# Kernel optimization log

Hardware: AMD Instinct MI355X
Metric: run time of the kernel (lower is better)

Reference implementation:

```python
import jax, jax.numpy as jnp
import numpy as np

N, E, B_GRAPHS = 50000, 512000, 64
XD, ED, C, H, L = 16, 8, 64, 2, 2
EPS = 1e-5


def setup_inputs() -> dict:
    key = jax.random.key(0)
    ks = jax.random.split(key, 20)
    w = lambda k, shape: jax.random.normal(k, shape, jnp.float32) * 0.1
    return {
        "x": jax.random.normal(ks[0], (N, XD), jnp.float32),
        "edge_attr": jax.random.normal(ks[1], (E, ED), jnp.float32),
        "edge_src": jax.random.randint(ks[2], (E,), 0, N, dtype=jnp.int32),
        "edge_dst": jax.random.randint(ks[3], (E,), 0, N, dtype=jnp.int32),
        "batch": jnp.sort(jax.random.randint(ks[4], (N,), 0, B_GRAPHS, dtype=jnp.int32)),
        "node_W": w(ks[5], (XD, C)), "node_b": jnp.zeros((C,), jnp.float32),
        "edge_W": w(ks[6], (ED, C)), "edge_b": jnp.zeros((C,), jnp.float32),
        "Wq": w(ks[7], (L, C, H * C)), "bq": jnp.zeros((L, H * C), jnp.float32),
        "Wk": w(ks[8], (L, C, H * C)), "bk": jnp.zeros((L, H * C), jnp.float32),
        "Wv": w(ks[9], (L, C, H * C)), "bv": jnp.zeros((L, H * C), jnp.float32),
        "We": w(ks[10], (L, C, H * C)), "be": jnp.zeros((L, H * C), jnp.float32),
        "Wskip": w(ks[11], (L, C, C)), "bskip": jnp.zeros((L, C), jnp.float32),
        "gamma": jnp.ones((L, C), jnp.float32), "beta": jnp.zeros((L, C), jnp.float32),
        "gate_W": w(ks[12], (C, 1)), "gate_b": jnp.zeros((1,), jnp.float32),
        "out_W": w(ks[13], (C, 1)), "out_b": jnp.zeros((1,), jnp.float32),
    }


def reference(x, edge_attr, edge_src, edge_dst, batch,
              node_W, node_b, edge_W, edge_b,
              Wq, bq, Wk, bk, Wv, bv, We, be,
              Wskip, bskip, gamma, beta,
              gate_W, gate_b, out_W, out_b):
    n = x.shape[0]
    h = x @ node_W + node_b                       # node encoder: [N, C]
    e = edge_attr @ edge_W + edge_b               # edge encoder: [E, C]
    scale = 1.0 / jnp.sqrt(jnp.float32(C))
    for i in range(L):
        identity = h
        # TransformerConv (UniMP), concat=False -> mean over heads
        q = (h @ Wq[i] + bq[i]).reshape(n, H, C)
        k = (h @ Wk[i] + bk[i]).reshape(n, H, C)
        v = (h @ Wv[i] + bv[i]).reshape(n, H, C)
        ep = (e @ We[i] + be[i]).reshape(-1, H, C)
        k_e = k[edge_src] + ep                    # [E, H, C]
        v_e = v[edge_src] + ep                    # [E, H, C]
        logits = jnp.einsum('ehc,ehc->eh', q[edge_dst], k_e) * scale
        # segment softmax over incoming edges of each target node
        m = jax.ops.segment_max(logits, edge_dst, num_segments=n)
        a = jnp.exp(logits - m[edge_dst])
        denom = jax.ops.segment_sum(a, edge_dst, num_segments=n)
        alpha = a / denom[edge_dst]               # [E, H]
        agg = jax.ops.segment_sum(alpha[:, :, None] * v_e, edge_dst, num_segments=n)
        out = agg.mean(axis=1) + h @ Wskip[i] + bskip[i]   # root/skip term
        # BatchNorm1d (training mode, biased variance)
        mu = out.mean(axis=0)
        var = out.var(axis=0)
        out = gamma[i] * (out - mu) * jax.lax.rsqrt(var + EPS) + beta[i]
        out = jax.nn.leaky_relu(out, 0.01)
        h = out + identity                        # residual
    # GlobalAttention pooling over graphs
    gate = (h @ gate_W + gate_b)[:, 0]            # [N]
    gm = jax.ops.segment_max(gate, batch, num_segments=B_GRAPHS)
    ge = jnp.exp(gate - gm[batch])
    gd = jax.ops.segment_sum(ge, batch, num_segments=B_GRAPHS)
    wts = ge / gd[batch]
    pooled = jax.ops.segment_sum(wts[:, None] * h, batch, num_segments=B_GRAPHS)
    return jax.nn.sigmoid(pooled @ out_W + out_b)  # [B_GRAPHS, 1]
```

## Files before the change

kernel.cpp:

```cpp
#include <hip/hip_runtime.h>
#include <hip/hip_bf16.h>

typedef unsigned short ushort_t;
typedef __attribute__((ext_vector_type(8))) short short8;
typedef __attribute__((ext_vector_type(4))) float float4v;

__device__ __forceinline__ float bfu_lo(unsigned u) {
    return __uint_as_float(u << 16);
}
__device__ __forceinline__ float bfu_hi(unsigned u) {
    return __uint_as_float(u & 0xffff0000u);
}
__device__ __forceinline__ ushort_t f2bf(float f) {
    __hip_bfloat16 h = __float2bfloat16(f);
    return *reinterpret_cast<ushort_t*>(&h);
}



__global__ __launch_bounds__(256) void setup_kernel(
    const float* __restrict__ x, const float* __restrict__ node_W,
    const float* __restrict__ node_b,
    const float* __restrict__ edge_W, const float* __restrict__ edge_b,
    const float* __restrict__ We, const float* __restrict__ be,
    const float* __restrict__ Wq, const float* __restrict__ bq,
    const float* __restrict__ Wk, const float* __restrict__ bk,
    const float* __restrict__ Wv, const float* __restrict__ bv,
    const float* __restrict__ Wskip, const float* __restrict__ bskip,
    float* __restrict__ h, ushort_t* __restrict__ h_bf,
    int* __restrict__ counts,
    float* __restrict__ Wc, float* __restrict__ bcb,
    ushort_t* __restrict__ Wall_arr, float* __restrict__ Wall_bias,
    ushort_t* __restrict__ wv_arr,
    int O0, int O1, int O2, int N) {
    int b = blockIdx.x, t = threadIdx.x;
    if (b < O0) {
        int idx = b * 256 + t;
        if (idx < N * 64) {
            int n = idx >> 6, c = idx & 63;
            float acc = node_b[c];
#pragma unroll
            for (int j = 0; j < 16; ++j) acc += x[n * 16 + j] * node_W[j * 64 + c];
            h[idx] = acc;
            h_bf[idx] = f2bf(acc);
        }
    } else if (b < O1) {
        int i = (b - O0) * 256 + t;
        if (i < N) counts[i] = 0;
    } else if (b < O2) {
        int tid = (b - O1) * 256 + t;
        if (tid < 2048) {
            int l = tid >> 10, d = (tid >> 7) & 7, j = tid & 127;
            float s = 0.f;
            for (int m = 0; m < 64; ++m) s += edge_W[d * 64 + m] * We[l * 8192 + m * 128 + j];
            Wc[l * 1024 + d * 128 + j] = s;
        } else if (tid < 2048 + 256) {
            int u = tid - 2048;
            int l = u >> 7, j = u & 127;
            float s = be[l * 128 + j];
            for (int m = 0; m < 64; ++m) s += edge_b[m] * We[l * 8192 + m * 128 + j];
            bcb[l * 128 + j] = s;
        }
    } else {
        int tid = (b - O2) * 256 + t;
        if (tid < 2 * 14336) {
            int l = tid / 14336, u = tid % 14336;
            int j = u & 7, ln = (u >> 3) & 63, kch = (u >> 9) & 1, ct = u >> 10;
            int nn = ln & 15, quad = ln >> 4;
            int k = kch * 32 + quad * 8 + j;
            int col = ct * 16 + nn;
            float v = 0.f;
            if (col < 128) {
                int hh = col >> 6, m = col & 63;
                const float* wq = Wq + l * 8192 + k * 128 + hh * 64;
                const float* wk = Wk + l * 8192 + m * 128 + hh * 64;
                float s = 0.f;
                for (int c2 = 0; c2 < 64; ++c2) s += wq[c2] * wk[c2];
                v = 0.125f * s;
            } else if (col < 192) {
                v = Wskip[l * 4096 + k * 64 + (col - 128)];
            }
            Wall_arr[(size_t)l * 14336 + ct * 1024 + kch * 512 + ln * 8 + j] = f2bf(v);
        } else if (tid < 2 * 14336 + 2 * 224) {
            int u = tid - 2 * 14336;
            int l = u / 224, col = u % 224;
            float v = 0.f;
            if (col < 128) {
                int hh = col >> 6, m = col & 63;
                const float* bqp = bq + l * 128 + hh * 64;
                const float* wk = Wk + l * 8192 + m * 128 + hh * 64;
                float s = 0.f;
                for (int c2 = 0; c2 < 64; ++c2) s += bqp[c2] * wk[c2];
                v = 0.125f * s;
            } else if (col < 192) {
                v = bskip[l * 64 + col - 128];
            }
            Wall_bias[l * 224 + col] = v;
        } else if (tid < 2 * 14336 + 2 * 224 + 2 * 8192) {
            int u = tid - (2 * 14336 + 2 * 224);
            int l = u >> 13, r = u & 8191;
            int j = r & 7, ln = (r >> 3) & 63, ct = (r >> 9) & 3, kc = r >> 11;
            int quad = ln >> 4, nn = ln & 15;
            int p = kc * 32 + quad * 8 + j;
            int hh = p >> 6, m = p & 63;
            int c2 = ct * 16 + nn;
            wv_arr[(size_t)l * 8192 + r] = f2bf(Wv[l * 8192 + m * 128 + hh * 64 + c2]);
        }
    }
}

__global__ void combine2_kernel(const float* __restrict__ Wq, const float* __restrict__ bq,
                                const float* __restrict__ bk, const float* __restrict__ bv,
                                const float* __restrict__ Wc, const float* __restrict__ bcb,
                                ushort_t* __restrict__ Wall_arr, float* __restrict__ Wall_bias,
                                float* __restrict__ cst) {
    int tid = blockIdx.x * 256 + threadIdx.x;
    if (tid < 2304) {
        int l = tid / 1152, u = tid % 1152, k = u / 18, j = u % 18;
        float s = 0.f;
        if (j < 16) {
            int hh = j >> 3, d = j & 7;
            for (int c = 0; c < 64; ++c)
                s += Wq[l * 8192 + k * 128 + hh * 64 + c] * Wc[l * 1024 + d * 128 + hh * 64 + c];
        } else {
            int hh = j - 16;
            for (int c = 0; c < 64; ++c)
                s += Wq[l * 8192 + k * 128 + hh * 64 + c] *
                     (bcb[l * 128 + hh * 64 + c] + bk[l * 128 + hh * 64 + c]);
        }
        s *= 0.125f;
        int col = 192 + j;
        int ct = col >> 4, nn = col & 15;
        int kch = k >> 5, quad = (k >> 3) & 3, jj = k & 7;
        int ln = quad * 16 + nn;
        Wall_arr[(size_t)l * 14336 + ct * 1024 + kch * 512 + ln * 8 + jj] = f2bf(s);
    } else if (tid < 2304 + 36) {
        int u = tid - 2304;
        int l = u / 18, j = u % 18;
        float s = 0.f;
        if (j < 16) {
            int hh = j >> 3, d = j & 7;
            for (int c = 0; c < 64; ++c)
                s += bq[l * 128 + hh * 64 + c] * Wc[l * 1024 + d * 128 + hh * 64 + c];
        } else {
            int hh = j - 16;
            for (int c = 0; c < 64; ++c)
                s += bq[l * 128 + hh * 64 + c] *
                     (bcb[l * 128 + hh * 64 + c] + bk[l * 128 + hh * 64 + c]);
        }
        Wall_bias[l * 224 + 192 + j] = 0.125f * s;
    } else if (tid < 2304 + 36 + 128) {
        int u = tid - 2340;
        int l = u >> 6, c = u & 63;
        cst[l * 64 + c] = 0.5f * (bv[l * 128 + c] + bv[l * 128 + 64 + c] +
                                  bcb[l * 128 + c] + bcb[l * 128 + 64 + c]);
    }
}


__global__ void csr_count_kernel(const int* __restrict__ dst, int* __restrict__ counts, int E) {
    int e = blockIdx.x * 256 + threadIdx.x;
    if (e < E) atomicAdd(&counts[dst[e]], 1);
}

__global__ void scan1_kernel(const int* __restrict__ counts, int* __restrict__ rowptr,
                             int* __restrict__ bsums, int N) {
    __shared__ int s[256];
    int t = threadIdx.x, i = blockIdx.x * 256 + t;
    int v = (i < N) ? counts[i] : 0;
    s[t] = v;
    __syncthreads();
    for (int d = 1; d < 256; d <<= 1) {
        int x = (t >= d) ? s[t - d] : 0;
        __syncthreads();
        s[t] += x;
        __syncthreads();
    }
    if (i < N) rowptr[i] = s[t] - v;
    if (t == 255) bsums[blockIdx.x] = s[255];
}

__global__ void scan3_kernel(int* __restrict__ rowptr, const int* __restrict__ bsums,
                             int* __restrict__ cursor, int N, int E, int nb) {
    __shared__ int sh[256];
    int t = threadIdx.x;
    int v = (t < nb) ? bsums[t] : 0;
    sh[t] = v;
    __syncthreads();
    for (int d = 1; d < 256; d <<= 1) {
        int x = (t >= d) ? sh[t - d] : 0;
        __syncthreads();
        sh[t] += x;
        __syncthreads();
    }
    int blk = blockIdx.x;
    int offv = (blk == 0) ? 0 : sh[blk - 1];
    int i = blk * 256 + t;
    if (i < N) {
        int r = rowptr[i] + offv;
        rowptr[i] = r;
        cursor[i] = r;
    }
    if (i == 0) rowptr[N] = E;
}

__global__ void csr_fill_kernel(const int* __restrict__ dst, const int* __restrict__ src,
                                const float* __restrict__ edge_attr, int* __restrict__ cursor,
                                char* __restrict__ erec, int E) {
    int e = blockIdx.x * 256 + threadIdx.x;
    if (e < E) {
        int pos = atomicAdd(&cursor[dst[e]], 1);
        float4 a0 = *(const float4*)(edge_attr + (size_t)e * 8);
        float4 a1 = *(const float4*)(edge_attr + (size_t)e * 8 + 4);
        uint4 w1;
        w1.x = (unsigned)f2bf(a0.x) | ((unsigned)f2bf(a0.y) << 16);
        w1.y = (unsigned)f2bf(a0.z) | ((unsigned)f2bf(a0.w) << 16);
        w1.z = (unsigned)f2bf(a1.x) | ((unsigned)f2bf(a1.y) << 16);
        w1.w = (unsigned)f2bf(a1.z) | ((unsigned)f2bf(a1.w) << 16);
        char* rp = erec + (size_t)pos * 32;
        *(uint4*)rp = make_uint4((unsigned)(src[e] * 128), 0u, 0u, 0u);
        *(uint4*)(rp + 16) = w1;
    }
}


__global__ __launch_bounds__(512) void layer_kernel(
    const ushort_t* __restrict__ h_bf,
    const char* __restrict__ erec, const int* __restrict__ rowptr,
    const ushort_t* __restrict__ Wall_arr, const float* __restrict__ Wall_bias,
    const ushort_t* __restrict__ wv_arr, const float* __restrict__ Wc,
    const float* __restrict__ cst,
    float* __restrict__ outbuf, float* __restrict__ part, int N) {
    __shared__ ushort_t qk2_s[32][128];
    __shared__ ushort_t ha_s[32][136];
    __shared__ float qc_s[32][20];
    __shared__ float skip_s[32][64];
    __shared__ float sen_s[32][16];
    __shared__ float dw_s[32];
    __shared__ float Wc_s[1024];
    __shared__ float cst_s[64];
    __shared__ float ps[2][128];
    int t = threadIdx.x;
    int lane = t & 63, wid = t >> 6;
    int n0 = blockIdx.x * 32;
    for (int i = t; i < 1024; i += 512) Wc_s[i] = Wc[i];
    if (t < 64) cst_s[t] = cst[t];

    {
        int quad = lane >> 4, nn16 = lane & 15;
        int nodeA = n0 + nn16;      if (nodeA >= N) nodeA = N - 1;
        int nodeB = n0 + 16 + nn16; if (nodeB >= N) nodeB = N - 1;
        const ushort_t* apA = h_bf + (size_t)nodeA * 64 + quad * 8;
        const ushort_t* apB = h_bf + (size_t)nodeB * 64 + quad * 8;
        short8 aA0 = *(const short8*)apA;
        short8 aA1 = *(const short8*)(apA + 32);
        short8 aB0 = *(const short8*)apB;
        short8 aB1 = *(const short8*)(apB + 32);
        for (int ct = wid; ct < 14; ct += 8) {
            const ushort_t* bp = Wall_arr + (size_t)ct * 1024 + lane * 8;
            short8 b0 = *(const short8*)bp;
            short8 b1 = *(const short8*)(bp + 512);
            float4v cA = {0.f, 0.f, 0.f, 0.f};
            float4v cB = {0.f, 0.f, 0.f, 0.f};
            cA = __builtin_amdgcn_mfma_f32_16x16x32_bf16(aA0, b0, cA, 0, 0, 0);
            cA = __builtin_amdgcn_mfma_f32_16x16x32_bf16(aA1, b1, cA, 0, 0, 0);
            cB = __builtin_amdgcn_mfma_f32_16x16x32_bf16(aB0, b0, cB, 0, 0, 0);
            cB = __builtin_amdgcn_mfma_f32_16x16x32_bf16(aB1, b1, cB, 0, 0, 0);
            int col = ct * 16 + nn16;
            float bias = Wall_bias[col];
#pragma unroll
            for (int g = 0; g < 2; ++g) {
                float4v c = g ? cB : cA;
                int lbase = g * 16 + quad * 4;
#pragma unroll
                for (int r = 0; r < 4; ++r) {
                    float v = c[r] + bias;
                    int ln2 = lbase + r;
                    if (col < 128) qk2_s[ln2][col] = f2bf(v);
                    else if (col < 192) skip_s[ln2][col - 128] = v;
                    else if (col < 210) qc_s[ln2][col - 192] = v;
                }
            }
        }
    }
    __syncthreads();

    {
        int grp = lane >> 4, l16 = lane & 15;
        int head = l16 >> 3, l8 = l16 & 7;
        const char* hbb = (const char*)h_bf;
        int ln = wid * 4 + grp;
        int n = n0 + ln;
        bool active = (n < N);
        int nn = active ? n : (N - 1);
        int start = rowptr[nn];
        int deg = active ? (rowptr[nn + 1] - start) : 0;
        int wdeg = deg;
        wdeg = max(wdeg, __shfl_xor(wdeg, 16));
        wdeg = max(wdeg, __shfl_xor(wdeg, 32));

        float lsum = 0.f;
        float hacc[8] = {0.f, 0.f, 0.f, 0.f, 0.f, 0.f, 0.f, 0.f};
        float se[8]   = {0.f, 0.f, 0.f, 0.f, 0.f, 0.f, 0.f, 0.f};

        if (wdeg > 0) {
            uint4 qr = *(const uint4*)&qk2_s[ln][head * 64 + l8 * 8];
            float qk0 = bfu_lo(qr.x), qk1 = bfu_hi(qr.x);
            float qk2f = bfu_lo(qr.y), qk3 = bfu_hi(qr.y);
            float qk4 = bfu_lo(qr.z), qk5 = bfu_hi(qr.z);
            float qk6 = bfu_lo(qr.w), qk7 = bfu_hi(qr.w);
            float4 qcA = *(const float4*)&qc_s[ln][head * 8];
            float4 qcB = *(const float4*)&qc_s[ln][head * 8 + 4];
            float qb = qc_s[ln][16 + head];

            bool dpos = (deg > 0);
            int dclamp = dpos ? (deg - 1) : 0;

            int offL = *(const int*)(erec + (size_t)(dpos ? (start + min(l16, dclamp)) : 0) * 32);
            int o0 = __shfl(offL, grp * 16);
            uint4 ca = *(const uint4*)(hbb + (size_t)(unsigned)o0 + l8 * 16);
            int gi0 = dpos ? start : 0;
            uint4 ev = *(const uint4*)(erec + (size_t)gi0 * 32 + 16);

            for (int it = 0; it < wdeg; ++it) {
                int itn = it + 1;
                if ((itn & 15) == 0)
                    offL = *(const int*)(erec +
                            (size_t)(dpos ? (start + min(itn + l16, dclamp)) : 0) * 32);
                int itc = min(itn, wdeg - 1);
                int on = __shfl(offL, grp * 16 + (itc & 15));
                uint4 na = *(const uint4*)(hbb + (size_t)(unsigned)on + l8 * 16);
                int gin = dpos ? (start + min(itc, dclamp)) : 0;
                uint4 fv = *(const uint4*)(erec + (size_t)gin * 32 + 16);

                float h0 = bfu_lo(ca.x), h1 = bfu_hi(ca.x);
                float h2 = bfu_lo(ca.y), h3 = bfu_hi(ca.y);
                float h4 = bfu_lo(ca.z), h5 = bfu_hi(ca.z);
                float h6 = bfu_lo(ca.w), h7 = bfu_hi(ca.w);
                float dt = qk0 * h0 + qk1 * h1 + qk2f * h2 + qk3 * h3
                         + qk4 * h4 + qk5 * h5 + qk6 * h6 + qk7 * h7;
                dt += __shfl_xor(dt, 1);
                dt += __shfl_xor(dt, 2);
                dt += __shfl_xor(dt, 4);
                float ex0 = bfu_lo(ev.x), ex1 = bfu_hi(ev.x);
                float ex2 = bfu_lo(ev.y), ex3 = bfu_hi(ev.y);
                float ex4 = bfu_lo(ev.z), ex5 = bfu_hi(ev.z);
                float ex6 = bfu_lo(ev.w), ex7 = bfu_hi(ev.w);
                float s0 = dt
                         + qcA.x * ex0 + qcA.y * ex1 + qcA.z * ex2 + qcA.w * ex3
                         + qcB.x * ex4 + qcB.y * ex5 + qcB.z * ex6 + qcB.w * ex7
                         + qb;
                float p = (it < deg) ? __expf(fmaxf(s0, -60.f)) : 0.f;
                lsum += p;
                hacc[0] += p * h0; hacc[1] += p * h1;
                hacc[2] += p * h2; hacc[3] += p * h3;
                hacc[4] += p * h4; hacc[5] += p * h5;
                hacc[6] += p * h6; hacc[7] += p * h7;
                se[0] += p * ex0; se[1] += p * ex1; se[2] += p * ex2; se[3] += p * ex3;
                se[4] += p * ex4; se[5] += p * ex5; se[6] += p * ex6; se[7] += p * ex7;
                ca = na; ev = fv;
            }
        }

        float inv = (deg > 0) ? (0.5f / lsum) : 0.f;
#pragma unroll
        for (int j2 = 0; j2 < 8; ++j2)
            ha_s[ln][head * 64 + l8 * 8 + j2] = f2bf(hacc[j2] * inv);
        if (l8 == 0) {
#pragma unroll
            for (int m = 0; m < 8; ++m) sen_s[ln][head * 8 + m] = se[m] * inv;
            if (head == 0) dw_s[ln] = (deg > 0) ? 1.f : 0.f;
        }
    }
    __syncthreads();

    {
        int quad = lane >> 4, nn16 = lane & 15;
        int ct = wid & 3, g = wid >> 2;
        float4v c = {0.f, 0.f, 0.f, 0.f};
#pragma unroll
        for (int kc = 0; kc < 4; ++kc) {
            short8 a = *(const short8*)&ha_s[g * 16 + nn16][kc * 32 + quad * 8];
            short8 b = *(const short8*)(wv_arr + kc * 2048 + ct * 512 + lane * 8);
            c = __builtin_amdgcn_mfma_f32_16x16x32_bf16(a, b, c, 0, 0, 0);
        }
        int col = ct * 16 + nn16;
        float sa = 0.f, sq = 0.f;
#pragma unroll
        for (int r = 0; r < 4; ++r) {
            int ln2 = g * 16 + quad * 4 + r;
            int nr = n0 + ln2;
            const float* sp = sen_s[ln2];
            float ep = 0.f;
#pragma unroll
            for (int hh = 0; hh < 2; ++hh)
#pragma unroll
                for (int d = 0; d < 8; ++d)
                    ep += sp[hh * 8 + d] * Wc_s[d * 128 + hh * 64 + col];
            if (nr < N) {
                float val = c[r] + ep + dw_s[ln2] * cst_s[col] + skip_s[ln2][col];
                outbuf[(size_t)nr * 64 + col] = val;
                sa += val;
                sq += val * val;
            }
        }
        sa += __shfl_xor(sa, 16); sa += __shfl_xor(sa, 32);
        sq += __shfl_xor(sq, 16); sq += __shfl_xor(sq, 32);
        if (quad == 0) { ps[g][col] = sa; ps[g][64 + col] = sq; }
    }
    __syncthreads();
    if (t < 128) part[(size_t)blockIdx.x * 128 + t] = ps[0][t] + ps[1][t];
}


__global__ __launch_bounds__(256) void bnreduce_kernel(const float* __restrict__ part,
                                                       float* __restrict__ bnsums, int nb) {
    int s = blockIdx.x;
    int t = threadIdx.x;
    float a = 0.f;
    for (int b = t; b < nb; b += 256) a += part[(size_t)b * 128 + s];
    __shared__ float sh[256];
    sh[t] = a;
    __syncthreads();
    for (int d = 128; d; d >>= 1) {
        if (t < d) sh[t] += sh[t + d];
        __syncthreads();
    }
    if (t == 0) bnsums[s] = sh[0];
}

__global__ __launch_bounds__(256) void bnh_kernel(
    const float* __restrict__ outbuf, const float* __restrict__ bnsums,
    const float* __restrict__ gamma, const float* __restrict__ beta,
    float* __restrict__ h, ushort_t* __restrict__ h_bf, int N) {
    int idx = blockIdx.x * 256 + threadIdx.x;
    if (idx >= N * 64) return;
    int c = idx & 63;
    float invN = 1.f / (float)N;
    float mean = bnsums[c] * invN;
    float var = bnsums[64 + c] * invN - mean * mean;
    float scale = gamma[c] * rsqrtf(var + 1e-5f);
    float shift = beta[c] - mean * scale;
    float o = outbuf[idx] * scale + shift;
    o = (o > 0.f) ? o : 0.01f * o;
    float hn = h[idx] + o;
    h[idx] = hn;
    h_bf[idx] = f2bf(hn);
}

__global__ __launch_bounds__(256) void bnapply_kernel(
    const float* __restrict__ outbuf, const float* __restrict__ bnsums,
    const float* __restrict__ gamma, const float* __restrict__ beta,
    const float* __restrict__ gate_W, const float* __restrict__ gate_b,
    float* __restrict__ h, float* __restrict__ gatebuf, int N) {
    int idx = blockIdx.x * 256 + threadIdx.x;
    if (idx >= N * 64) return;
    int c = idx & 63, n = idx >> 6;
    float invN = 1.f / (float)N;
    float mean = bnsums[c] * invN;
    float var = bnsums[64 + c] * invN - mean * mean;
    float scale = gamma[c] * rsqrtf(var + 1e-5f);
    float shift = beta[c] - mean * scale;
    float o = outbuf[idx] * scale + shift;
    o = (o > 0.f) ? o : 0.01f * o;
    float hn = h[idx] + o;
    h[idx] = hn;
    float g = hn * gate_W[c];
#pragma unroll
    for (int off = 32; off; off >>= 1) g += __shfl_xor(g, off);
    if (c == 0) gatebuf[n] = g + gate_b[0];
}


__global__ __launch_bounds__(256) void pool_acc_kernel(
    const float* __restrict__ h, const float* __restrict__ gatebuf,
    const int* __restrict__ batch,
    float* __restrict__ pacc, float* __restrict__ pden, int N) {
    int b = blockIdx.x >> 3, chunk = blockIdx.x & 7;
    int lo = 0, hi = N;
    while (lo < hi) { int mid = (lo + hi) >> 1; if (batch[mid] < b) lo = mid + 1; else hi = mid; }
    int start = lo;
    lo = start; hi = N;
    while (lo < hi) { int mid = (lo + hi) >> 1; if (batch[mid] <= b) lo = mid + 1; else hi = mid; }
    int end = lo;
    int t = threadIdx.x, lane = t & 63, wid = t >> 6;
    __shared__ float sm[4];
    float mx = -1e30f;
    for (int n = start + t; n < end; n += 256) mx = fmaxf(mx, gatebuf[n]);
#pragma unroll
    for (int off = 32; off; off >>= 1) mx = fmaxf(mx, __shfl_xor(mx, off));
    if (lane == 0) sm[wid] = mx;
    __syncthreads();
    float mb = fmaxf(fmaxf(sm[0], sm[1]), fmaxf(sm[2], sm[3]));
    int gwid = chunk * 4 + wid;
    float acc = 0.f, den = 0.f;
    for (int n = start + gwid; n < end; n += 32) {
        float ge = __expf(gatebuf[n] - mb);
        acc += ge * h[(size_t)n * 64 + lane];
        den += ge;
    }
    __shared__ float sacc[4][64];
    __shared__ float sden[4];
    sacc[wid][lane] = acc;
    if (lane == 0) sden[wid] = den;
    __syncthreads();
    if (wid == 0) {
        pacc[(size_t)blockIdx.x * 64 + lane] =
            sacc[0][lane] + sacc[1][lane] + sacc[2][lane] + sacc[3][lane];
        if (lane == 0) pden[blockIdx.x] = sden[0] + sden[1] + sden[2] + sden[3];
    }
}

__global__ void pool_fin_kernel(const float* __restrict__ pacc, const float* __restrict__ pden,
                                const float* __restrict__ out_W, const float* __restrict__ out_b,
                                float* __restrict__ out) {
    int b = blockIdx.x, c = threadIdx.x;
    float pc = 0.f, dv = 0.f;
#pragma unroll
    for (int j = 0; j < 8; ++j) {
        pc += pacc[(size_t)(b * 8 + j) * 64 + c];
        dv += pden[b * 8 + j];
    }
    float s = pc * out_W[c];
#pragma unroll
    for (int off = 32; off; off >>= 1) s += __shfl_xor(s, off);
    if (c == 0) {
        if (dv <= 0.f) dv = 1.f;
        float v = s / dv + out_b[0];
        out[b] = 1.f / (1.f + __expf(-v));
    }
}


extern "C" void kernel_launch(void* const* d_in, const int* in_sizes, int n_in,
                              void* d_out, int out_size, void* d_ws, size_t ws_size,
                              hipStream_t stream) {
    const float* x         = (const float*)d_in[0];
    const float* edge_attr = (const float*)d_in[1];
    const int*   edge_src  = (const int*)d_in[2];
    const int*   edge_dst  = (const int*)d_in[3];
    const int*   batch     = (const int*)d_in[4];
    const float* node_W    = (const float*)d_in[5];
    const float* node_b    = (const float*)d_in[6];
    const float* edge_W    = (const float*)d_in[7];
    const float* edge_b    = (const float*)d_in[8];
    const float* Wq        = (const float*)d_in[9];
    const float* bq        = (const float*)d_in[10];
    const float* Wk        = (const float*)d_in[11];
    const float* bk        = (const float*)d_in[12];
    const float* Wv        = (const float*)d_in[13];
    const float* bv        = (const float*)d_in[14];
    const float* We        = (const float*)d_in[15];
    const float* be        = (const float*)d_in[16];
    const float* Wskip     = (const float*)d_in[17];
    const float* bskip     = (const float*)d_in[18];
    const float* gamma     = (const float*)d_in[19];
    const float* beta      = (const float*)d_in[20];
    const float* gate_W    = (const float*)d_in[21];
    const float* gate_b    = (const float*)d_in[22];
    const float* out_W     = (const float*)d_in[23];
    const float* out_b     = (const float*)d_in[24];
    float* out = (float*)d_out;

    const int N = in_sizes[0] / 16;
    const int E = in_sizes[2];
    const int nbv = (N + 31) / 32;

    char* ws = (char*)d_ws;
    size_t off = 0;
    auto alloc = [&](size_t bytes) {
        size_t o = off;
        off += (bytes + 255) & ~(size_t)255;
        return o;
    };
    float*    h        = (float*)(ws + alloc((size_t)N * 64 * 4));
    ushort_t* h_bf     = (ushort_t*)(ws + alloc((size_t)N * 64 * 2));
    float*    outbuf   = (float*)(ws + alloc((size_t)N * 64 * 4));
    int*      rowptr   = (int*)(ws + alloc((size_t)(N + 1) * 4));
    int*      cursor   = (int*)(ws + alloc((size_t)N * 4));
    int*      counts   = (int*)(ws + alloc((size_t)N * 4));
    int*      bsums    = (int*)(ws + alloc(1024));
    char*     erec     = (char*)(ws + alloc((size_t)E * 32));
    float*    Wc       = (float*)(ws + alloc(2 * 1024 * 4));
    float*    bcb      = (float*)(ws + alloc(2 * 128 * 4));
    ushort_t* Wall_arr = (ushort_t*)(ws + alloc(2 * 14336 * 2));
    float*    Wall_b   = (float*)(ws + alloc(2 * 224 * 4));
    ushort_t* wv_arr   = (ushort_t*)(ws + alloc(2 * 8192 * 2));
    float*    cst      = (float*)(ws + alloc(2 * 64 * 4));
    float*    bnsums   = (float*)(ws + alloc(128 * 4));
    float*    gatebuf  = (float*)(ws + alloc((size_t)N * 4));
    float*    part     = (float*)(ws + alloc((size_t)nbv * 128 * 4));
    float*    pacc     = (float*)(ws + alloc((size_t)512 * 64 * 4));
    float*    pden     = (float*)(ws + alloc(512 * 4));
    if (off > ws_size) return;

    int O0 = (N * 64 + 255) / 256;
    int O1 = O0 + (N + 255) / 256;
    int O2 = O1 + 9;
    int O3 = O2 + 178;
    setup_kernel<<<O3, 256, 0, stream>>>(
        x, node_W, node_b, edge_W, edge_b, We, be, Wq, bq, Wk, bk, Wv, bv, Wskip, bskip,
        h, h_bf, counts, Wc, bcb, Wall_arr, Wall_b, wv_arr, O0, O1, O2, N);
    combine2_kernel<<<10, 256, 0, stream>>>(Wq, bq, bk, bv, Wc, bcb, Wall_arr, Wall_b, cst);

    csr_count_kernel<<<(E + 255) / 256, 256, 0, stream>>>(edge_dst, counts, E);
    int nb = (N + 255) / 256;
    scan1_kernel<<<nb, 256, 0, stream>>>(counts, rowptr, bsums, N);
    scan3_kernel<<<nb, 256, 0, stream>>>(rowptr, bsums, cursor, N, E, nb);
    csr_fill_kernel<<<(E + 255) / 256, 256, 0, stream>>>(edge_dst, edge_src, edge_attr,
                                                         cursor, erec, E);

    layer_kernel<<<nbv, 512, 0, stream>>>(h_bf, erec, rowptr,
                                          Wall_arr, Wall_b, wv_arr, Wc, cst,
                                          outbuf, part, N);
    bnreduce_kernel<<<128, 256, 0, stream>>>(part, bnsums, nbv);
    bnh_kernel<<<(N * 64 + 255) / 256, 256, 0, stream>>>(
        outbuf, bnsums, gamma, beta, h, h_bf, N);

    layer_kernel<<<nbv, 512, 0, stream>>>(h_bf, erec, rowptr,
                                          Wall_arr + 14336, Wall_b + 224, wv_arr + 8192,
                                          Wc + 1024, cst + 64,
                                          outbuf, part, N);
    bnreduce_kernel<<<128, 256, 0, stream>>>(part, bnsums, nbv);
    bnapply_kernel<<<(N * 64 + 255) / 256, 256, 0, stream>>>(
        outbuf, bnsums, gamma + 64, beta + 64, gate_W, gate_b, h, gatebuf, N);

    pool_acc_kernel<<<512, 256, 0, stream>>>(h, gatebuf, batch, pacc, pden, N);
    pool_fin_kernel<<<64, 64, 0, stream>>>(pacc, pden, out_W, out_b, out);
}
```

Baseline: 341.5 us.

## Split each node's incoming edges across two warps, halving nodes per block

The layer kernel now handles 16 nodes per 512-thread block instead of 32, and each node's edge list is split between a pair of wavefronts. Each half accumulates partial softmax sums and weighted features, which are merged through shared memory before normalization. This shortens the serial per-node edge loop, evens out load across degrees, and doubles the block count. The cost is an extra barrier and shared-memory reduction, less reuse of the projection weights per block, and only half the waves taking part in the final MFMA stage.

```diff
diff --git a/kernel.cpp b/kernel.cpp
--- a/kernel.cpp
+++ b/kernel.cpp
@@ -231,55 +231,46 @@
     const ushort_t* __restrict__ wv_arr, const float* __restrict__ Wc,
     const float* __restrict__ cst,
     float* __restrict__ outbuf, float* __restrict__ part, int N) {
-    __shared__ ushort_t qk2_s[32][128];
-    __shared__ ushort_t ha_s[32][136];
-    __shared__ float qc_s[32][20];
-    __shared__ float skip_s[32][64];
-    __shared__ float sen_s[32][16];
-    __shared__ float dw_s[32];
+    __shared__ ushort_t qk2_s[16][128];
+    __shared__ ushort_t ha_s[16][136];
+    __shared__ float qc_s[16][20];
+    __shared__ float skip_s[16][64];
+    __shared__ float sen_s[16][16];
+    __shared__ float dw_s[16];
     __shared__ float Wc_s[1024];
     __shared__ float cst_s[64];
-    __shared__ float ps[2][128];
+    __shared__ float ps[128];
+    __shared__ float ph[16][128];
+    __shared__ float pse[16][16];
+    __shared__ float plsum[16][2];
     int t = threadIdx.x;
     int lane = t & 63, wid = t >> 6;
-    int n0 = blockIdx.x * 32;
+    int n0 = blockIdx.x * 16;
     for (int i = t; i < 1024; i += 512) Wc_s[i] = Wc[i];
     if (t < 64) cst_s[t] = cst[t];
 
     {
         int quad = lane >> 4, nn16 = lane & 15;
-        int nodeA = n0 + nn16;      if (nodeA >= N) nodeA = N - 1;
-        int nodeB = n0 + 16 + nn16; if (nodeB >= N) nodeB = N - 1;
+        int nodeA = n0 + nn16; if (nodeA >= N) nodeA = N - 1;
         const ushort_t* apA = h_bf + (size_t)nodeA * 64 + quad * 8;
-        const ushort_t* apB = h_bf + (size_t)nodeB * 64 + quad * 8;
         short8 aA0 = *(const short8*)apA;
         short8 aA1 = *(const short8*)(apA + 32);
-        short8 aB0 = *(const short8*)apB;
-        short8 aB1 = *(const short8*)(apB + 32);
         for (int ct = wid; ct < 14; ct += 8) {
             const ushort_t* bp = Wall_arr + (size_t)ct * 1024 + lane * 8;
             short8 b0 = *(const short8*)bp;
             short8 b1 = *(const short8*)(bp + 512);
             float4v cA = {0.f, 0.f, 0.f, 0.f};
-            float4v cB = {0.f, 0.f, 0.f, 0.f};
             cA = __builtin_amdgcn_mfma_f32_16x16x32_bf16(aA0, b0, cA, 0, 0, 0);
             cA = __builtin_amdgcn_mfma_f32_16x16x32_bf16(aA1, b1, cA, 0, 0, 0);
-            cB = __builtin_amdgcn_mfma_f32_16x16x32_bf16(aB0, b0, cB, 0, 0, 0);
-            cB = __builtin_amdgcn_mfma_f32_16x16x32_bf16(aB1, b1, cB, 0, 0, 0);
             int col = ct * 16 + nn16;
             float bias = Wall_bias[col];
 #pragma unroll
-            for (int g = 0; g < 2; ++g) {
-                float4v c = g ? cB : cA;
-                int lbase = g * 16 + quad * 4;
-#pragma unroll
-                for (int r = 0; r < 4; ++r) {
-                    float v = c[r] + bias;
-                    int ln2 = lbase + r;
-                    if (col < 128) qk2_s[ln2][col] = f2bf(v);
-                    else if (col < 192) skip_s[ln2][col - 128] = v;
-                    else if (col < 210) qc_s[ln2][col - 192] = v;
-                }
+            for (int r = 0; r < 4; ++r) {
+                float v = cA[r] + bias;
+                int ln2 = quad * 4 + r;
+                if (col < 128) qk2_s[ln2][col] = f2bf(v);
+                else if (col < 192) skip_s[ln2][col - 128] = v;
+                else if (col < 210) qc_s[ln2][col - 192] = v;
             }
         }
     }
@@ -288,14 +279,18 @@
     {
         int grp = lane >> 4, l16 = lane & 15;
         int head = l16 >> 3, l8 = l16 & 7;
+        int pairIdx = wid >> 1, halfIdx = wid & 1;
         const char* hbb = (const char*)h_bf;
-        int ln = wid * 4 + grp;
+        int ln = pairIdx * 4 + grp;
         int n = n0 + ln;
         bool active = (n < N);
         int nn = active ? n : (N - 1);
         int start = rowptr[nn];
         int deg = active ? (rowptr[nn + 1] - start) : 0;
-        int wdeg = deg;
+        int h1cnt = (deg + 1) >> 1;
+        int mycnt = halfIdx ? (deg - h1cnt) : h1cnt;
+        int mystart = start + (halfIdx ? h1cnt : 0);
+        int wdeg = mycnt;
         wdeg = max(wdeg, __shfl_xor(wdeg, 16));
         wdeg = max(wdeg, __shfl_xor(wdeg, 32));
 
@@ -313,24 +308,23 @@
             float4 qcB = *(const float4*)&qc_s[ln][head * 8 + 4];
             float qb = qc_s[ln][16 + head];
 
-            bool dpos = (deg > 0);
-            int dclamp = dpos ? (deg - 1) : 0;
-
-            int offL = *(const int*)(erec + (size_t)(dpos ? (start + min(l16, dclamp)) : 0) * 32);
+            bool dpos = (mycnt > 0);
+            int dclamp = dpos ? (mycnt - 1) : 0;
+            int base = dpos ? mystart : 0;
+
+            int offL = *(const int*)(erec + (size_t)(base + min(l16, dclamp)) * 32);
             int o0 = __shfl(offL, grp * 16);
             uint4 ca = *(const uint4*)(hbb + (size_t)(unsigned)o0 + l8 * 16);
-            int gi0 = dpos ? start : 0;
-            uint4 ev = *(const uint4*)(erec + (size_t)gi0 * 32 + 16);
+            uint4 ev = *(const uint4*)(erec + (size_t)base * 32 + 16);
 
             for (int it = 0; it < wdeg; ++it) {
                 int itn = it + 1;
                 if ((itn & 15) == 0)
-                    offL = *(const int*)(erec +
-                            (size_t)(dpos ? (start + min(itn + l16, dclamp)) : 0) * 32);
+                    offL = *(const int*)(erec + (size_t)(base + min(itn + l16, dclamp)) * 32);
                 int itc = min(itn, wdeg - 1);
                 int on = __shfl(offL, grp * 16 + (itc & 15));
                 uint4 na = *(const uint4*)(hbb + (size_t)(unsigned)on + l8 * 16);
-                int gin = dpos ? (start + min(itc, dclamp)) : 0;
+                int gin = base + min(itc, dclamp);
                 uint4 fv = *(const uint4*)(erec + (size_t)gin * 32 + 16);
 
                 float h0 = bfu_lo(ca.x), h1 = bfu_hi(ca.x);
@@ -350,7 +344,7 @@
                          + qcA.x * ex0 + qcA.y * ex1 + qcA.z * ex2 + qcA.w * ex3
                          + qcB.x * ex4 + qcB.y * ex5 + qcB.z * ex6 + qcB.w * ex7
                          + qb;
-                float p = (it < deg) ? __expf(fmaxf(s0, -60.f)) : 0.f;
+                float p = (it < mycnt) ? __expf(fmaxf(s0, -60.f)) : 0.f;
                 lsum += p;
                 hacc[0] += p * h0; hacc[1] += p * h1;
                 hacc[2] += p * h2; hacc[3] += p * h3;
@@ -362,25 +356,41 @@
             }
         }
 
-        float inv = (deg > 0) ? (0.5f / lsum) : 0.f;
-#pragma unroll
-        for (int j2 = 0; j2 < 8; ++j2)
-            ha_s[ln][head * 64 + l8 * 8 + j2] = f2bf(hacc[j2] * inv);
-        if (l8 == 0) {
-#pragma unroll
-            for (int m = 0; m < 8; ++m) sen_s[ln][head * 8 + m] = se[m] * inv;
-            if (head == 0) dw_s[ln] = (deg > 0) ? 1.f : 0.f;
-        }
-    }
-    __syncthreads();
-
-    {
+        if (halfIdx == 1) {
+#pragma unroll
+            for (int j2 = 0; j2 < 8; ++j2) ph[ln][head * 64 + l8 * 8 + j2] = hacc[j2];
+            if (l8 == 0) {
+#pragma unroll
+                for (int m = 0; m < 8; ++m) pse[ln][head * 8 + m] = se[m];
+                plsum[ln][head] = lsum;
+            }
+        }
+        __syncthreads();
+        if (halfIdx == 0) {
+            lsum += plsum[ln][head];
+#pragma unroll
+            for (int j2 = 0; j2 < 8; ++j2) hacc[j2] += ph[ln][head * 64 + l8 * 8 + j2];
+            float inv = (deg > 0) ? (0.5f / lsum) : 0.f;
+#pragma unroll
+            for (int j2 = 0; j2 < 8; ++j2)
+                ha_s[ln][head * 64 + l8 * 8 + j2] = f2bf(hacc[j2] * inv);
+            if (l8 == 0) {
+#pragma unroll
+                for (int m = 0; m < 8; ++m)
+                    sen_s[ln][head * 8 + m] = (se[m] + pse[ln][head * 8 + m]) * inv;
+                if (head == 0) dw_s[ln] = (deg > 0) ? 1.f : 0.f;
+            }
+        }
+    }
+    __syncthreads();
+
+    if (wid < 4) {
         int quad = lane >> 4, nn16 = lane & 15;
-        int ct = wid & 3, g = wid >> 2;
+        int ct = wid;
         float4v c = {0.f, 0.f, 0.f, 0.f};
 #pragma unroll
         for (int kc = 0; kc < 4; ++kc) {
-            short8 a = *(const short8*)&ha_s[g * 16 + nn16][kc * 32 + quad * 8];
+            short8 a = *(const short8*)&ha_s[nn16][kc * 32 + quad * 8];
             short8 b = *(const short8*)(wv_arr + kc * 2048 + ct * 512 + lane * 8);
             c = __builtin_amdgcn_mfma_f32_16x16x32_bf16(a, b, c, 0, 0, 0);
         }
@@ -388,7 +398,7 @@
         float sa = 0.f, sq = 0.f;
 #pragma unroll
         for (int r = 0; r < 4; ++r) {
-            int ln2 = g * 16 + quad * 4 + r;
+            int ln2 = quad * 4 + r;
             int nr = n0 + ln2;
             const float* sp = sen_s[ln2];
             float ep = 0.f;
@@ -406,10 +416,10 @@
         }
         sa += __shfl_xor(sa, 16); sa += __shfl_xor(sa, 32);
         sq += __shfl_xor(sq, 16); sq += __shfl_xor(sq, 32);
-        if (quad == 0) { ps[g][col] = sa; ps[g][64 + col] = sq; }
-    }
-    __syncthreads();
-    if (t < 128) part[(size_t)blockIdx.x * 128 + t] = ps[0][t] + ps[1][t];
+        if (quad == 0) { ps[col] = sa; ps[64 + col] = sq; }
+    }
+    __syncthreads();
+    if (t < 128) part[(size_t)blockIdx.x * 128 + t] = ps[t];
 }
 
 
@@ -564,7 +574,7 @@
 
     const int N = in_sizes[0] / 16;
     const int E = in_sizes[2];
-    const int nbv = (N + 31) / 32;
+    const int nbl = (N + 15) / 16;
 
     char* ws = (char*)d_ws;
     size_t off = 0;
@@ -589,7 +599,7 @@
     float*    cst      = (float*)(ws + alloc(2 * 64 * 4));
     float*    bnsums   = (float*)(ws + alloc(128 * 4));
     float*    gatebuf  = (float*)(ws + alloc((size_t)N * 4));
-    float*    part     = (float*)(ws + alloc((size_t)nbv * 128 * 4));
+    float*    part     = (float*)(ws + alloc((size_t)nbl * 128 * 4));
     float*    pacc     = (float*)(ws + alloc((size_t)512 * 64 * 4));
     float*    pden     = (float*)(ws + alloc(512 * 4));
     if (off > ws_size) return;
@@ -610,18 +620,18 @@
     csr_fill_kernel<<<(E + 255) / 256, 256, 0, stream>>>(edge_dst, edge_src, edge_attr,
                                                          cursor, erec, E);
 
-    layer_kernel<<<nbv, 512, 0, stream>>>(h_bf, erec, rowptr,
+    layer_kernel<<<nbl, 512, 0, stream>>>(h_bf, erec, rowptr,
                                           Wall_arr, Wall_b, wv_arr, Wc, cst,
                                           outbuf, part, N);
-    bnreduce_kernel<<<128, 256, 0, stream>>>(part, bnsums, nbv);
+    bnreduce_kernel<<<128, 256, 0, stream>>>(part, bnsums, nbl);
     bnh_kernel<<<(N * 64 + 255) / 256, 256, 0, stream>>>(
         outbuf, bnsums, gamma, beta, h, h_bf, N);
 
-    layer_kernel<<<nbv, 512, 0, stream>>>(h_bf, erec, rowptr,
+    layer_kernel<<<nbl, 512, 0, stream>>>(h_bf, erec, rowptr,
                                           Wall_arr + 14336, Wall_b + 224, wv_arr + 8192,
                                           Wc + 1024, cst + 64,
                                           outbuf, part, N);
-    bnreduce_kernel<<<128, 256, 0, stream>>>(part, bnsums, nbv);
+    bnreduce_kernel<<<128, 256, 0, stream>>>(part, bnsums, nbl);
     bnapply_kernel<<<(N * 64 + 255) / 256, 256, 0, stream>>>(
         outbuf, bnsums, gamma + 64, beta + 64, gate_W, gate_b, h, gatebuf, N);
 
```

Result: slower. 358.5 us (+5.0%).
